# Optimization experiments

Measured on AMD Instinct MI355X. Metric: run time of the kernel, lower is better.

## Reference

```python
import jax, jax.numpy as jnp
import numpy as np

NEG_INF = -1e30


def setup_inputs() -> dict:
    key = jax.random.key(0)
    k1, k2 = jax.random.split(key)
    N, Q, M = 8, 2048, 2048
    gen_adj = jax.random.normal(k1, (N, Q, M), dtype=jnp.float32)
    # per-sample k in [1, 64]; force one sample to the max so topknum is deterministic
    topk = jax.random.randint(k2, (N, 1), 1, 65, dtype=jnp.int64)
    topk = topk.at[0, 0].set(64)
    return {"gen_adj": gen_adj, "topk": topk}


def reference(gen_adj, topk):
    # gen_adj: [N, Q, M] float, topk: [N, 1] int (per-sample variable k)
    N, Q, M = gen_adj.shape
    k_per = jnp.minimum(topk, M)                      # clamp like min(topk[i], M)
    topknum = int(jnp.max(k_per))                     # padded output width

    a = jnp.abs(gen_adj)                              # [N, Q, M]
    vals, idx = jax.lax.top_k(a, topknum)             # [N, Q, K] each (sorted desc)

    pos = jnp.arange(topknum)                         # [K]
    valid = pos[None, None, :] < k_per[:, :, None]    # [N, 1, K] -> broadcasts over Q

    # softmax over only the first k_i logits per sample; padded slots -> 0
    logits = jnp.where(valid, vals, NEG_INF)
    r_weight = jax.nn.softmax(logits, axis=-1)
    r_weight = jnp.where(valid, r_weight, 0.0)        # exact zeros in padding
    topk_index = jnp.where(valid, idx, 0)             # pad indices with 0
    return r_weight, topk_index
```

## Files before the change

### kernel.cpp

```cpp
#include <hip/hip_runtime.h>

#define M_COLS 2048
#define KOUT 64
#define CAND 128
#define BLK 256

typedef unsigned long long u64;

#define DPPU(old, src, ctrl, rmask) \
  ((unsigned)__builtin_amdgcn_update_dpp((int)(old), (int)(src), (ctrl), (rmask), 0xF, false))
#define RDL(x, l) ((unsigned)__builtin_amdgcn_readlane((int)(x), (l)))

#define SCAN_ADD_U(x)             \
  do {                            \
    x += DPPU(0u, x, 0x111, 0xF); \
    x += DPPU(0u, x, 0x112, 0xF); \
    x += DPPU(0u, x, 0x114, 0xF); \
    x += DPPU(0u, x, 0x118, 0xF); \
    x += DPPU(0u, x, 0x142, 0xA); \
    x += DPPU(0u, x, 0x143, 0xC); \
  } while (0)

#define SCAN_MAX_U(x)                                  \
  do {                                                 \
    unsigned _t;                                       \
    _t = DPPU(0u, x, 0x111, 0xF); x = x > _t ? x : _t; \
    _t = DPPU(0u, x, 0x112, 0xF); x = x > _t ? x : _t; \
    _t = DPPU(0u, x, 0x114, 0xF); x = x > _t ? x : _t; \
    _t = DPPU(0u, x, 0x118, 0xF); x = x > _t ? x : _t; \
    _t = DPPU(0u, x, 0x142, 0xA); x = x > _t ? x : _t; \
    _t = DPPU(0u, x, 0x143, 0xC); x = x > _t ? x : _t; \
  } while (0)

#define SCAN_ADD_F(x)                                               \
  do {                                                              \
    x += __uint_as_float(DPPU(0u, __float_as_uint(x), 0x111, 0xF)); \
    x += __uint_as_float(DPPU(0u, __float_as_uint(x), 0x112, 0xF)); \
    x += __uint_as_float(DPPU(0u, __float_as_uint(x), 0x114, 0xF)); \
    x += __uint_as_float(DPPU(0u, __float_as_uint(x), 0x118, 0xF)); \
    x += __uint_as_float(DPPU(0u, __float_as_uint(x), 0x142, 0xA)); \
    x += __uint_as_float(DPPU(0u, __float_as_uint(x), 0x143, 0xC)); \
  } while (0)

#define SWZ(v, J) ((unsigned)__builtin_amdgcn_ds_swizzle((int)(v), (((J) << 10) | 0x1f)))

#define EX_S(dst, src, J)                           \
  do {                                              \
    unsigned _lo = SWZ((unsigned)(src), J);         \
    unsigned _hi = SWZ((unsigned)((src) >> 32), J); \
    dst = ((u64)_hi << 32) | _lo;                   \
  } while (0)
#define EX_D(dst, src, CTRL)                                     \
  do {                                                           \
    unsigned _lo = DPPU(0u, (unsigned)(src), CTRL, 0xF);         \
    unsigned _hi = DPPU(0u, (unsigned)((src) >> 32), CTRL, 0xF); \
    dst = ((u64)_hi << 32) | _lo;                                \
  } while (0)
#define EX_W(dst, src)                                                         \
  do {                                                                         \
    unsigned _lo = (unsigned)__shfl_xor((int)(unsigned)(src), 32, 64);         \
    unsigned _hi = (unsigned)__shfl_xor((int)(unsigned)((src) >> 32), 32, 64); \
    dst = ((u64)_hi << 32) | _lo;                                              \
  } while (0)

#define CMPSEL(up)                       \
  do {                                   \
    k0 = ((k0 >= o0) == (up)) ? k0 : o0; \
    k1 = ((k1 >= o1) == (up)) ? o1 : k1; \
  } while (0)

#define STEP_A_S(J, UP) do { u64 o0, o1; EX_S(o0, k0, J); EX_S(o1, k1, J); CMPSEL(UP); } while (0)
#define STEP_A_D(CTRL, UP) do { u64 o0, o1; EX_D(o0, k0, CTRL); EX_D(o1, k1, CTRL); CMPSEL(UP); } while (0)
#define STEP_A_W(UP) do { u64 o0, o1; EX_W(o0, k0); EX_W(o1, k1); CMPSEL(UP); } while (0)

#define STEP_B_S(J, UP) do { u64 o; EX_S(o, av, J); av = ((av >= o) == (UP)) ? av : o; } while (0)
#define STEP_B_D(CTRL, UP) do { u64 o; EX_D(o, av, CTRL); av = ((av >= o) == (UP)) ? av : o; } while (0)
#define STEP_B_W(UP) do { u64 o; EX_W(o, av); av = ((av >= o) == (UP)) ? av : o; } while (0)

__global__ __launch_bounds__(BLK) void topk_route_kernel(
    const float* __restrict__ A, const int* __restrict__ topk,
    float* __restrict__ out_w, float* __restrict__ out_i, int NQ, int Q, int N) {
  __shared__ u64 cand[4][CAND];

  const unsigned tid = threadIdx.x;
  const unsigned wv = tid >> 6, lane = tid & 63u;
  const unsigned row = blockIdx.x * 4u + wv;
  if ((int)row >= NQ) return;
  const unsigned n = row / (unsigned)Q;

  const float4* a4 = (const float4*)(A + (size_t)row * M_COLS);
  unsigned bits[32];
#pragma unroll
  for (int t = 0; t < 8; ++t) {
    float4 vv = a4[lane + 64u * (unsigned)t];
    bits[4 * t + 0] = __float_as_uint(vv.x) & 0x7fffffffu;
    bits[4 * t + 1] = __float_as_uint(vv.y) & 0x7fffffffu;
    bits[4 * t + 2] = __float_as_uint(vv.z) & 0x7fffffffu;
    bits[4 * t + 3] = __float_as_uint(vv.w) & 0x7fffffffu;
  }

  cand[wv][lane + 64u] = 0ull;

  int kk;
  if (N >= 8) {
    const int4* t4 = (const int4*)topk;
    int4 a = t4[0], b = t4[1], c = t4[2], d = t4[3];
    int k64 = topk[2 * (int)n], k32 = topk[(int)n];
    bool looks64 = (a.y == 0) & (a.w == 0) & (b.y == 0) & (b.w == 0) &
                   (c.y == 0) & (c.w == 0) & (d.y == 0) & (d.w == 0) &
                   (a.x >= 1) & (a.z >= 1) & (b.x >= 1) & (b.z >= 1) &
                   (c.x >= 1) & (c.z >= 1) & (d.x >= 1) & (d.z >= 1);
    kk = looks64 ? k64 : k32;
  } else {
    bool looks64 = true;
    for (int i = 0; i < N; ++i) {
      int l = topk[2 * i], h = topk[2 * i + 1];
      if (h != 0 || l < 1) { looks64 = false; break; }
    }
    kk = looks64 ? topk[2 * (int)n] : topk[(int)n];
  }
  kk = kk > M_COLS ? M_COLS : (kk < 0 ? 0 : kk);

  unsigned keep = 0u, sl = 0u, inc = 0u, csel = 0u;
  auto attempt = [&](unsigned T) {
    unsigned q0 = 0u, q1 = 0u, q2 = 0u, q3 = 0u;
#pragma unroll
    for (int j = 7; j >= 0; --j) {
      q0 = q0 + q0 + (unsigned)(bits[j] >= T);
      q1 = q1 + q1 + (unsigned)(bits[8 + j] >= T);
      q2 = q2 + q2 + (unsigned)(bits[16 + j] >= T);
      q3 = q3 + q3 + (unsigned)(bits[24 + j] >= T);
    }
    keep = q0 | (q1 << 8) | (q2 << 16) | (q3 << 24);
    sl = __popc(keep);
    inc = sl;
    SCAN_ADD_U(inc);
    csel = RDL(inc, 63);
  };

  attempt(0x40000000u);

  if (csel < KOUT || csel > CAND) {
    unsigned mx = bits[0];
#pragma unroll
    for (int j = 1; j < 32; ++j) mx = bits[j] > mx ? bits[j] : mx;
    SCAN_MAX_U(mx);
    mx = RDL(mx, 63);
    const int em = (int)(mx >> 23);

    unsigned lo, hi = mx + 1u;
    {
      unsigned T = (em > 0) ? ((unsigned)em << 23) : 0u;
      attempt(T); lo = T;
      if (csel < KOUT) {
        hi = T;
        T = (em - 1 > 0) ? ((unsigned)(em - 1) << 23) : 0u;
        attempt(T); lo = T;
        if (csel < KOUT) {
          hi = T;
          T = (em - 2 > 0) ? ((unsigned)(em - 2) << 23) : 0u;
          attempt(T); lo = T;
          if (csel < KOUT) { hi = T; attempt(0u); lo = 0u; }
        }
      }
    }

    {
      unsigned csel_lo = csel, lastT = lo;
      while (csel_lo > CAND && lo + 1u < hi) {
        unsigned mid = lo + ((hi - lo) >> 1);
        attempt(mid); lastT = mid;
        if (csel >= KOUT) { lo = mid; csel_lo = csel; } else hi = mid;
      }
      if (lastT != lo) attempt(lo);
    }

    if (csel > CAND) {
      unsigned kgt = 0u;
#pragma unroll
      for (int j = 31; j >= 0; --j) kgt = (kgt << 1) | (unsigned)(bits[j] >= hi);
      unsigned slgt = __popc(kgt), incgt = slgt;
      SCAN_ADD_U(incgt);
      unsigned cgt = RDL(incgt, 63);
      unsigned cap = CAND - cgt;
      keep = kgt;
      unsigned run = 0u;
#pragma unroll
      for (int t = 0; t < 8; ++t) {
        unsigned f = 0u;
#pragma unroll
        for (int c = 3; c >= 0; --c) f = (f << 1) | (unsigned)(bits[4 * t + c] == lo);
        unsigned tc = __popc(f), it = tc;
        SCAN_ADD_U(it);
        unsigned tbase = run + it - tc;
#pragma unroll
        for (int c = 0; c < 4; ++c) {
          if (f & (1u << c)) {
            if (tbase < cap) keep |= 1u << (4 * t + c);
            ++tbase;
          }
        }
        run += RDL(it, 63);
      }
      sl = __popc(keep);
      inc = sl;
      SCAN_ADD_U(inc);
      csel = RDL(inc, 63);
    }
  }

  unsigned base = inc - sl;
  const unsigned lobase = 2047u - 4u * lane;
  u64* cw = &cand[wv][0];
#pragma unroll
  for (int j = 0; j < 32; ++j) {
    if (keep & (1u << j)) {
      unsigned pj = base + (unsigned)__popc(keep & ((1u << j) - 1u));
      cw[pj] = ((u64)bits[j] << 32) |
               (u64)(lobase - (unsigned)((j >> 2) * 256 + (j & 3)));
    }
  }

  const bool b1 = (lane & 1u) != 0u, b2 = (lane & 2u) != 0u, b4 = (lane & 4u) != 0u;
  const bool b8 = (lane & 8u) != 0u, b16 = (lane & 16u) != 0u, b32 = (lane & 32u) != 0u;

  u64 k0 = cw[lane];
  u64 k1 = cw[lane + 64u];
  STEP_A_D(0xB1, !(b2 ^ b1));
  STEP_A_D(0x4E, !(b4 ^ b2)); STEP_A_D(0xB1, !(b4 ^ b1));
  STEP_A_S(4, !(b8 ^ b4)); STEP_A_D(0x4E, !(b8 ^ b2)); STEP_A_D(0xB1, !(b8 ^ b1));
  STEP_A_S(8, !(b16 ^ b8)); STEP_A_S(4, !(b16 ^ b4));
  STEP_A_D(0x4E, !(b16 ^ b2)); STEP_A_D(0xB1, !(b16 ^ b1));
  STEP_A_S(16, !(b32 ^ b16)); STEP_A_S(8, !(b32 ^ b8)); STEP_A_S(4, !(b32 ^ b4));
  STEP_A_D(0x4E, !(b32 ^ b2)); STEP_A_D(0xB1, !(b32 ^ b1));
  STEP_A_W(!b32);
  STEP_A_S(16, !b16); STEP_A_S(8, !b8); STEP_A_S(4, !b4);
  STEP_A_D(0x4E, !b2); STEP_A_D(0xB1, !b1);

  u64 av = k0 >= k1 ? k0 : k1;
  STEP_B_W(!b32);
  STEP_B_S(16, !b16); STEP_B_S(8, !b8); STEP_B_S(4, !b4);
  STEP_B_D(0x4E, !b2); STEP_B_D(0xB1, !b1);

  float val = __uint_as_float((unsigned)(av >> 32));
  unsigned midx = 2047u - (unsigned)(av & 0xffffffffull);
  bool valid = (int)lane < kk;

  float vmx = __uint_as_float(
      (unsigned)__builtin_amdgcn_readfirstlane((int)(unsigned)(av >> 32)));
  float e = valid ? __expf(val - vmx) : 0.0f;
  float s = e;
  SCAN_ADD_F(s);
  float stot = __uint_as_float(RDL(__float_as_uint(s), 63));
  float w = valid ? (e / stot) : 0.0f;

  size_t o = (size_t)row * KOUT + lane;
  out_w[o] = w;
  out_i[o] = valid ? (float)midx : 0.0f;
}

extern "C" void kernel_launch(void* const* d_in, const int* in_sizes, int n_in,
                              void* d_out, int out_size, void* d_ws, size_t ws_size,
                              hipStream_t stream) {
  const float* A = (const float*)d_in[0];
  const int* topk = (const int*)d_in[1];
  float* out = (float*)d_out;
  const int NQ = in_sizes[0] / M_COLS;
  const int N = in_sizes[1] > 0 ? in_sizes[1] : 1;
  const int Q = NQ / N;
  float* out_w = out;
  float* out_i = out + (size_t)NQ * KOUT;
  const int blocks = (NQ + 3) / 4;
  hipLaunchKernelGGL(topk_route_kernel, dim3(blocks), dim3(BLK), 0, stream, A,
                     topk, out_w, out_i, NQ, Q, N);
}
```

Before: 29.78 us.

## Stream candidate compaction with ballot/mbcnt instead of register-held bitmasks

Drops the 32-register per-lane copy of the row. Candidates are now compacted straight from each float4 load, using wave ballots and mbcnt prefix counts in place of a bitmask plus a DPP prefix scan. The rare fallback threshold search now re-reads the row from global memory for each count rather than keeping it in registers. The aim is lower register pressure and fewer scan instructions on the common path, at the cost of extra global re-reads when the fixed threshold misses.

```diff
diff --git a/kernel.cpp b/kernel.cpp
--- a/kernel.cpp
+++ b/kernel.cpp
@@ -10,16 +10,6 @@
 #define DPPU(old, src, ctrl, rmask) \
   ((unsigned)__builtin_amdgcn_update_dpp((int)(old), (int)(src), (ctrl), (rmask), 0xF, false))
 #define RDL(x, l) ((unsigned)__builtin_amdgcn_readlane((int)(x), (l)))
-
-#define SCAN_ADD_U(x)             \
-  do {                            \
-    x += DPPU(0u, x, 0x111, 0xF); \
-    x += DPPU(0u, x, 0x112, 0xF); \
-    x += DPPU(0u, x, 0x114, 0xF); \
-    x += DPPU(0u, x, 0x118, 0xF); \
-    x += DPPU(0u, x, 0x142, 0xA); \
-    x += DPPU(0u, x, 0x143, 0xC); \
-  } while (0)
 
 #define SCAN_MAX_U(x)                                  \
   do {                                                 \
@@ -42,6 +32,10 @@
     x += __uint_as_float(DPPU(0u, __float_as_uint(x), 0x143, 0xC)); \
   } while (0)
 
+#define MB64(m)                                         \
+  __builtin_amdgcn_mbcnt_hi((unsigned)((m) >> 32),      \
+      __builtin_amdgcn_mbcnt_lo((unsigned)(m), 0u))
+
 #define SWZ(v, J) ((unsigned)__builtin_amdgcn_ds_swizzle((int)(v), (((J) << 10) | 0x1f)))
 
 #define EX_S(dst, src, J)                           \
@@ -89,17 +83,8 @@
   const unsigned n = row / (unsigned)Q;
 
   const float4* a4 = (const float4*)(A + (size_t)row * M_COLS);
-  unsigned bits[32];
-#pragma unroll
-  for (int t = 0; t < 8; ++t) {
-    float4 vv = a4[lane + 64u * (unsigned)t];
-    bits[4 * t + 0] = __float_as_uint(vv.x) & 0x7fffffffu;
-    bits[4 * t + 1] = __float_as_uint(vv.y) & 0x7fffffffu;
-    bits[4 * t + 2] = __float_as_uint(vv.z) & 0x7fffffffu;
-    bits[4 * t + 3] = __float_as_uint(vv.w) & 0x7fffffffu;
-  }
-
-  cand[wv][lane + 64u] = 0ull;
+  u64* cw = &cand[wv][0];
+  const unsigned lob = 2047u - 4u * lane;
 
   int kk;
   if (N >= 8) {
@@ -121,104 +106,117 @@
   }
   kk = kk > M_COLS ? M_COLS : (kk < 0 ? 0 : kk);
 
-  unsigned keep = 0u, sl = 0u, inc = 0u, csel = 0u;
-  auto attempt = [&](unsigned T) {
-    unsigned q0 = 0u, q1 = 0u, q2 = 0u, q3 = 0u;
-#pragma unroll
-    for (int j = 7; j >= 0; --j) {
-      q0 = q0 + q0 + (unsigned)(bits[j] >= T);
-      q1 = q1 + q1 + (unsigned)(bits[8 + j] >= T);
-      q2 = q2 + q2 + (unsigned)(bits[16 + j] >= T);
-      q3 = q3 + q3 + (unsigned)(bits[24 + j] >= T);
-    }
-    keep = q0 | (q1 << 8) | (q2 << 16) | (q3 << 24);
-    sl = __popc(keep);
-    inc = sl;
-    SCAN_ADD_U(inc);
-    csel = RDL(inc, 63);
+  unsigned base = 0u;
+  auto compact4 = [&](float4 vv, int t, unsigned T) {
+    unsigned b0 = __float_as_uint(vv.x) & 0x7fffffffu;
+    unsigned b1 = __float_as_uint(vv.y) & 0x7fffffffu;
+    unsigned b2 = __float_as_uint(vv.z) & 0x7fffffffu;
+    unsigned b3 = __float_as_uint(vv.w) & 0x7fffffffu;
+    bool p0 = b0 >= T, p1 = b1 >= T, p2 = b2 >= T, p3 = b3 >= T;
+    u64 m0 = __ballot(p0), m1 = __ballot(p1), m2 = __ballot(p2), m3 = __ballot(p3);
+    unsigned mba = MB64(m0) + MB64(m1) + MB64(m2) + MB64(m3);
+    unsigned l1 = (unsigned)p0, l2 = l1 + (unsigned)p1, l3 = l2 + (unsigned)p2;
+    unsigned pb = base + mba;
+    if (p0 && pb < CAND)      cw[pb]      = ((u64)b0 << 32) | (u64)(lob - (unsigned)(256 * t + 0));
+    if (p1 && pb + l1 < CAND) cw[pb + l1] = ((u64)b1 << 32) | (u64)(lob - (unsigned)(256 * t + 1));
+    if (p2 && pb + l2 < CAND) cw[pb + l2] = ((u64)b2 << 32) | (u64)(lob - (unsigned)(256 * t + 2));
+    if (p3 && pb + l3 < CAND) cw[pb + l3] = ((u64)b3 << 32) | (u64)(lob - (unsigned)(256 * t + 3));
+    base += (unsigned)__popcll(m0) + (unsigned)__popcll(m1) +
+            (unsigned)__popcll(m2) + (unsigned)__popcll(m3);
   };
 
-  attempt(0x40000000u);
-
-  if (csel < KOUT || csel > CAND) {
-    unsigned mx = bits[0];
-#pragma unroll
-    for (int j = 1; j < 32; ++j) mx = bits[j] > mx ? bits[j] : mx;
+  {
+    float4 v0 = a4[lane];          float4 v1 = a4[lane + 64u];
+    float4 v2 = a4[lane + 128u];   float4 v3 = a4[lane + 192u];
+    float4 v4 = a4[lane + 256u];   float4 v5 = a4[lane + 320u];
+    float4 v6 = a4[lane + 384u];   float4 v7 = a4[lane + 448u];
+    compact4(v0, 0, 0x40000000u);  compact4(v1, 1, 0x40000000u);
+    compact4(v2, 2, 0x40000000u);  compact4(v3, 3, 0x40000000u);
+    compact4(v4, 4, 0x40000000u);  compact4(v5, 5, 0x40000000u);
+    compact4(v6, 6, 0x40000000u);  compact4(v7, 7, 0x40000000u);
+  }
+
+  if (base < KOUT || base > CAND) {
+    auto count_ge = [&](unsigned T) -> unsigned {
+      unsigned c = 0u;
+      for (int t = 0; t < 8; ++t) {
+        float4 vv = a4[lane + 64u * (unsigned)t];
+        c += (unsigned)__popcll(__ballot((__float_as_uint(vv.x) & 0x7fffffffu) >= T));
+        c += (unsigned)__popcll(__ballot((__float_as_uint(vv.y) & 0x7fffffffu) >= T));
+        c += (unsigned)__popcll(__ballot((__float_as_uint(vv.z) & 0x7fffffffu) >= T));
+        c += (unsigned)__popcll(__ballot((__float_as_uint(vv.w) & 0x7fffffffu) >= T));
+      }
+      return c;
+    };
+
+    unsigned mx = 0u;
+    for (int t = 0; t < 8; ++t) {
+      float4 vv = a4[lane + 64u * (unsigned)t];
+      unsigned c0 = __float_as_uint(vv.x) & 0x7fffffffu;
+      unsigned c1 = __float_as_uint(vv.y) & 0x7fffffffu;
+      unsigned c2 = __float_as_uint(vv.z) & 0x7fffffffu;
+      unsigned c3 = __float_as_uint(vv.w) & 0x7fffffffu;
+      unsigned m01 = c0 > c1 ? c0 : c1, m23 = c2 > c3 ? c2 : c3;
+      unsigned mm = m01 > m23 ? m01 : m23;
+      mx = mm > mx ? mm : mx;
+    }
     SCAN_MAX_U(mx);
     mx = RDL(mx, 63);
     const int em = (int)(mx >> 23);
 
-    unsigned lo, hi = mx + 1u;
+    unsigned lo, hi = mx + 1u, csel;
     {
       unsigned T = (em > 0) ? ((unsigned)em << 23) : 0u;
-      attempt(T); lo = T;
+      csel = count_ge(T); lo = T;
       if (csel < KOUT) {
         hi = T;
         T = (em - 1 > 0) ? ((unsigned)(em - 1) << 23) : 0u;
-        attempt(T); lo = T;
+        csel = count_ge(T); lo = T;
         if (csel < KOUT) {
           hi = T;
           T = (em - 2 > 0) ? ((unsigned)(em - 2) << 23) : 0u;
-          attempt(T); lo = T;
-          if (csel < KOUT) { hi = T; attempt(0u); lo = 0u; }
+          csel = count_ge(T); lo = T;
+          if (csel < KOUT) { hi = T; lo = 0u; csel = count_ge(0u); }
         }
       }
     }
-
-    {
-      unsigned csel_lo = csel, lastT = lo;
-      while (csel_lo > CAND && lo + 1u < hi) {
-        unsigned mid = lo + ((hi - lo) >> 1);
-        attempt(mid); lastT = mid;
-        if (csel >= KOUT) { lo = mid; csel_lo = csel; } else hi = mid;
+    while (csel > CAND && lo + 1u < hi) {
+      unsigned mid = lo + ((hi - lo) >> 1);
+      unsigned c = count_ge(mid);
+      if (c >= KOUT) { lo = mid; csel = c; } else hi = mid;
+    }
+
+    base = 0u;
+    if (csel <= CAND) {
+      for (int t = 0; t < 8; ++t) compact4(a4[lane + 64u * (unsigned)t], t, lo);
+    } else {
+      for (int t = 0; t < 8; ++t) compact4(a4[lane + 64u * (unsigned)t], t, hi);
+      for (int t = 0; t < 8; ++t) {
+        float4 vv = a4[lane + 64u * (unsigned)t];
+        unsigned b0 = __float_as_uint(vv.x) & 0x7fffffffu;
+        unsigned b1 = __float_as_uint(vv.y) & 0x7fffffffu;
+        unsigned b2 = __float_as_uint(vv.z) & 0x7fffffffu;
+        unsigned b3 = __float_as_uint(vv.w) & 0x7fffffffu;
+        bool p0 = b0 == lo, p1 = b1 == lo, p2 = b2 == lo, p3 = b3 == lo;
+        u64 m0 = __ballot(p0), m1 = __ballot(p1), m2 = __ballot(p2), m3 = __ballot(p3);
+        unsigned mba = MB64(m0) + MB64(m1) + MB64(m2) + MB64(m3);
+        unsigned l1 = (unsigned)p0, l2 = l1 + (unsigned)p1, l3 = l2 + (unsigned)p2;
+        unsigned pb = base + mba;
+        if (p0 && pb < CAND)      cw[pb]      = ((u64)b0 << 32) | (u64)(lob - (unsigned)(256 * t + 0));
+        if (p1 && pb + l1 < CAND) cw[pb + l1] = ((u64)b1 << 32) | (u64)(lob - (unsigned)(256 * t + 1));
+        if (p2 && pb + l2 < CAND) cw[pb + l2] = ((u64)b2 << 32) | (u64)(lob - (unsigned)(256 * t + 2));
+        if (p3 && pb + l3 < CAND) cw[pb + l3] = ((u64)b3 << 32) | (u64)(lob - (unsigned)(256 * t + 3));
+        base += (unsigned)__popcll(m0) + (unsigned)__popcll(m1) +
+                (unsigned)__popcll(m2) + (unsigned)__popcll(m3);
       }
-      if (lastT != lo) attempt(lo);
-    }
-
-    if (csel > CAND) {
-      unsigned kgt = 0u;
-#pragma unroll
-      for (int j = 31; j >= 0; --j) kgt = (kgt << 1) | (unsigned)(bits[j] >= hi);
-      unsigned slgt = __popc(kgt), incgt = slgt;
-      SCAN_ADD_U(incgt);
-      unsigned cgt = RDL(incgt, 63);
-      unsigned cap = CAND - cgt;
-      keep = kgt;
-      unsigned run = 0u;
-#pragma unroll
-      for (int t = 0; t < 8; ++t) {
-        unsigned f = 0u;
-#pragma unroll
-        for (int c = 3; c >= 0; --c) f = (f << 1) | (unsigned)(bits[4 * t + c] == lo);
-        unsigned tc = __popc(f), it = tc;
-        SCAN_ADD_U(it);
-        unsigned tbase = run + it - tc;
-#pragma unroll
-        for (int c = 0; c < 4; ++c) {
-          if (f & (1u << c)) {
-            if (tbase < cap) keep |= 1u << (4 * t + c);
-            ++tbase;
-          }
-        }
-        run += RDL(it, 63);
-      }
-      sl = __popc(keep);
-      inc = sl;
-      SCAN_ADD_U(inc);
-      csel = RDL(inc, 63);
-    }
-  }
-
-  unsigned base = inc - sl;
-  const unsigned lobase = 2047u - 4u * lane;
-  u64* cw = &cand[wv][0];
-#pragma unroll
-  for (int j = 0; j < 32; ++j) {
-    if (keep & (1u << j)) {
-      unsigned pj = base + (unsigned)__popc(keep & ((1u << j) - 1u));
-      cw[pj] = ((u64)bits[j] << 32) |
-               (u64)(lobase - (unsigned)((j >> 2) * 256 + (j & 3)));
-    }
+      base = base > CAND ? CAND : base;
+    }
+  }
+
+  {
+    unsigned pz0 = base + lane, pz1 = base + 64u + lane;
+    if (pz0 < CAND) cw[pz0] = 0ull;
+    if (pz1 < CAND) cw[pz1] = 0ull;
   }
 
   const bool b1 = (lane & 1u) != 0u, b2 = (lane & 2u) != 0u, b4 = (lane & 4u) != 0u;
```

Measured after the change: 31.63 us. 1.06x slower.
